# Optimization experiments

Hardware: AMD Instinct MI355X
Metric: run time of the kernel (lower is better)

The kernel has to match this reference:

```python
import jax, jax.numpy as jnp
import numpy as np

EMBED_DIM = 1024
NUM_HEADS = 16
HEAD_DIM = EMBED_DIM // NUM_HEADS
B, S = 2, 2048


def setup_inputs() -> dict:
    key = jax.random.key(0)
    ks = jax.random.split(key, 9)
    d = EMBED_DIM
    scale = 1.0 / np.sqrt(d)
    inp = {
        "x": jax.random.normal(ks[0], (B, S, d), dtype=jnp.float32),
        "mask": jnp.ones((B, S), dtype=jnp.int32),
        "Wq": jax.random.normal(ks[1], (d, d), dtype=jnp.float32) * scale,
        "bq": jnp.zeros((d,), dtype=jnp.float32),
        "Wk": jax.random.normal(ks[2], (d, d), dtype=jnp.float32) * scale,
        "bk": jnp.zeros((d,), dtype=jnp.float32),
        "Wv": jax.random.normal(ks[3], (d, d), dtype=jnp.float32) * scale,
        "bv": jnp.zeros((d,), dtype=jnp.float32),
        "Wo": jax.random.normal(ks[4], (d, d), dtype=jnp.float32) * scale,
        "bo": jnp.zeros((d,), dtype=jnp.float32),
    }
    return inp


def reference(x, mask, Wq, bq, Wk, bk, Wv, bv, Wo, bo):
    b, s, _ = x.shape
    # projections; torch Linear computes x @ W.T + b
    q = (x @ Wq.T + bq).reshape(b, s, NUM_HEADS, HEAD_DIM).transpose(0, 2, 1, 3)
    k = (x @ Wk.T + bk).reshape(b, s, NUM_HEADS, HEAD_DIM).transpose(0, 2, 1, 3)
    v = (x @ Wv.T + bv).reshape(b, s, NUM_HEADS, HEAD_DIM).transpose(0, 2, 1, 3)
    scores = jnp.einsum("bhqd,bhkd->bhqk", q, k) / np.sqrt(HEAD_DIM)  # (B,H,S,S)
    m = (mask == 0)[:, None, None, :]  # broadcast over heads and query pos
    scores = jnp.where(m, jnp.float32(-1e9), scores)
    attn = jax.nn.softmax(scores, axis=-1)
    out = jnp.einsum("bhqk,bhkd->bhqd", attn, v)
    out = out.transpose(0, 2, 1, 3).reshape(b, s, EMBED_DIM)
    return out @ Wo.T + bo
```

## Files before the change

kernel.cpp:

```cpp
#include <hip/hip_runtime.h>

#define EMBED 1024
#define NHEAD 16
#define HDIM  64
#define BB    2
#define SS    2048

typedef __bf16 bf16x8 __attribute__((ext_vector_type(8)));
typedef float  f32x4  __attribute__((ext_vector_type(4)));
typedef _Float16 f16x8 __attribute__((ext_vector_type(8)));
typedef __fp16 hf16x2 __attribute__((ext_vector_type(2)));
typedef unsigned short u16x8 __attribute__((ext_vector_type(8)));

#if defined(__has_builtin)
#if __has_builtin(__builtin_amdgcn_exp2f)
#define EXP2(x) __builtin_amdgcn_exp2f(x)
#else
#define EXP2(x) exp2f(x)
#endif
#else
#define EXP2(x) exp2f(x)
#endif

__device__ __forceinline__ unsigned short f2bf(float f) {
  union { float f; unsigned u; } v; v.f = f;
  unsigned r = v.u + 0x7fffu + ((v.u >> 16) & 1u);
  return (unsigned short)(r >> 16);
}

__device__ __forceinline__ float bf2f(unsigned short u) {
  union { unsigned u; float f; } v; v.u = ((unsigned)u) << 16;
  return v.f;
}

__device__ __forceinline__ unsigned short f2h(float f) {
  union { _Float16 h; unsigned short u; } t;
  t.h = (_Float16)f;
  return t.u;
}

__device__ __forceinline__ void g2l16(const unsigned short* g, unsigned short* l) {
  __builtin_amdgcn_global_load_lds(
      (const __attribute__((address_space(1))) unsigned int*)g,
      (__attribute__((address_space(3))) unsigned int*)l, 16, 0, 0);
}

__global__ __launch_bounds__(256)
void cvt5_kernel(const float* __restrict__ x,  const float* __restrict__ Wq,
                 const float* __restrict__ Wk, const float* __restrict__ Wv,
                 const float* __restrict__ Wo, const int* __restrict__ mask,
                 unsigned short* __restrict__ xb,  unsigned short* __restrict__ Wqb,
                 unsigned short* __restrict__ Wkb, unsigned short* __restrict__ Wvb,
                 unsigned short* __restrict__ Wob, float* __restrict__ mbias) {
  const int i = blockIdx.x * 256 + threadIdx.x;
  if (i < (1 << 21)) {
    const float* src;
    unsigned short* dst;
    int j;
    if (i < (1 << 20)) {
      src = x; dst = xb; j = i;
    } else {
      const int t = i - (1 << 20);
      const int r = t >> 18;
      j = t & ((1 << 18) - 1);
      src = (r == 0) ? Wq : (r == 1) ? Wk : (r == 2) ? Wv : Wo;
      dst = (r == 0) ? Wqb : (r == 1) ? Wkb : (r == 2) ? Wvb : Wob;
    }
    const float4 f = ((const float4*)src)[j];
    ushort4 u;
    u.x = f2bf(f.x); u.y = f2bf(f.y); u.z = f2bf(f.z); u.w = f2bf(f.w);
    ((ushort4*)dst)[j] = u;
  } else {
    const int j = i - (1 << 21);
    const int4 m = ((const int4*)mask)[j];
    float4 o;
    o.x = m.x ? 0.f : -1e30f; o.y = m.y ? 0.f : -1e30f;
    o.z = m.z ? 0.f : -1e30f; o.w = m.w ? 0.f : -1e30f;
    ((float4*)mbias)[j] = o;
  }
}

template <typename EpiFn>
__device__ __forceinline__
void gemm_core(const unsigned short* __restrict__ A,
               const unsigned short* __restrict__ Bm,
               int m0, int n0, EpiFn epi) {
  __shared__ unsigned short sA[128 * 64];
  __shared__ unsigned short sB[128 * 64];
  const int tid = threadIdx.x;
  const int l  = tid & 63;
  const int w  = tid >> 6;
  const int lm = l & 15;
  const int qd = l >> 4;
  const int wm = w & 1;
  const int wn = w >> 1;

  f32x4 acc[4][4];
#pragma unroll
  for (int i = 0; i < 4; ++i)
#pragma unroll
    for (int j = 0; j < 4; ++j) acc[i][j] = (f32x4){0.f, 0.f, 0.f, 0.f};

  for (int k0 = 0; k0 < EMBED; k0 += 64) {
#pragma unroll
    for (int i = 0; i < 4; ++i) {
      const int t = i * 256 + tid;
      const int r = t >> 3;
      const int c = (t & 7) ^ (r & 7);
      g2l16(A + (m0 + r) * EMBED + k0 + c * 8, &sA[(i * 256 + (w << 6)) * 8]);
      g2l16(Bm + (n0 + r) * EMBED + k0 + c * 8, &sB[(i * 256 + (w << 6)) * 8]);
    }
    __syncthreads();
#pragma unroll
    for (int kk = 0; kk < 2; ++kk) {
      bf16x8 af[4], bfr[4];
#pragma unroll
      for (int mi = 0; mi < 4; ++mi) {
        const int R = wm * 64 + mi * 16 + lm;
        const int ch = R * 8 + (((kk << 2) + qd) ^ (R & 7));
        af[mi] = *(const bf16x8*)&sA[ch * 8];
      }
#pragma unroll
      for (int ni = 0; ni < 4; ++ni) {
        const int R = wn * 64 + ni * 16 + lm;
        const int ch = R * 8 + (((kk << 2) + qd) ^ (R & 7));
        bfr[ni] = *(const bf16x8*)&sB[ch * 8];
      }
#pragma unroll
      for (int mi = 0; mi < 4; ++mi)
#pragma unroll
        for (int ni = 0; ni < 4; ++ni)
          acc[mi][ni] = __builtin_amdgcn_mfma_f32_16x16x32_bf16(
              af[mi], bfr[ni], acc[mi][ni], 0, 0, 0);
    }
    __syncthreads();
  }

#pragma unroll
  for (int mi = 0; mi < 4; ++mi)
#pragma unroll
    for (int ni = 0; ni < 4; ++ni) {
      const int mb = m0 + wm * 64 + mi * 16 + qd * 4;
      const int n  = n0 + wn * 64 + ni * 16 + lm;
      epi(acc[mi][ni], mb, n);
    }
}

__device__ __forceinline__ void decode_tile(int flat, int& a0, int& b0) {
  const int sub = flat & 15;
  const int g = flat >> 4;
  a0 = ((g >> 2) * 2 + (sub >> 3));
  b0 = ((g & 3) * 8 + (sub & 7));
}

__global__ __launch_bounds__(256)
void gemm_qkv(const unsigned short* __restrict__ xb,
              const unsigned short* __restrict__ Wqb,
              const unsigned short* __restrict__ Wkb,
              const unsigned short* __restrict__ Wvb,
              const float* __restrict__ bq, const float* __restrict__ bk,
              const float* __restrict__ bv,
              unsigned short* __restrict__ Qb, unsigned short* __restrict__ Kb,
              unsigned short* __restrict__ VTb) {
  const int z = blockIdx.y;
  int a0, b0;
  decode_tile(blockIdx.x, a0, b0);
  if (z < 2) {
    const unsigned short* A = z ? Wkb : Wqb;
    const float* bias = z ? bk : bq;
    unsigned short* O = z ? Kb : Qb;
    const float scale = z ? 1.0f : 0.125f * 1.4426950408889634f;
    gemm_core(A, xb, a0 * 128, b0 * 128, [&](const f32x4& v, int mb, int n) {
      const float4 bvv = *(const float4*)&bias[mb];
      const int h = mb >> 6, d0 = mb & 63;
      const int b = n >> 11, s = n & 2047;
      int sw = s;
      if (z == 1)
        sw = (s & ~31) | (((s >> 2) & 1) << 4) | (((s >> 3) & 3) << 2) | (s & 3);
      ushort4 u;
      u.x = f2bf((v.x + bvv.x) * scale); u.y = f2bf((v.y + bvv.y) * scale);
      u.z = f2bf((v.z + bvv.z) * scale); u.w = f2bf((v.w + bvv.w) * scale);
      *(ushort4*)&O[(((b * NHEAD + h) * SS) + sw) * HDIM + d0] = u;
    });
  } else {
    gemm_core(xb, Wvb, b0 * 128, a0 * 128, [&](const f32x4& v, int mb, int n) {
      const float bvv = bv[n];
      const int b = mb >> 11, s = mb & 2047;
      const int h = n >> 6, d = n & 63;
      ushort4 u;
      u.x = f2h(v.x + bvv); u.y = f2h(v.y + bvv);
      u.z = f2h(v.z + bvv); u.w = f2h(v.w + bvv);
      *(ushort4*)&VTb[(((b * NHEAD + h) * HDIM) + d) * SS + s] = u;
    });
  }
}

__global__ __launch_bounds__(256)
void gemm_out(const unsigned short* __restrict__ Wob,
              const unsigned short* __restrict__ Opart,
              const float* __restrict__ Lpart,
              const float* __restrict__ bo, float* __restrict__ out) {
  __shared__ unsigned short sA[128 * 64];
  __shared__ unsigned short sB[128 * 64];
  int a0, b0;
  decode_tile(blockIdx.x, a0, b0);
  const int m0 = a0 * 128, n0 = b0 * 128;
  const int tid = threadIdx.x;
  const int l  = tid & 63;
  const int w  = tid >> 6;
  const int lm = l & 15;
  const int qd = l >> 4;
  const int wm = w & 1;
  const int wn = w >> 1;

  f32x4 acc[4][4];
#pragma unroll
  for (int i = 0; i < 4; ++i)
#pragma unroll
    for (int j = 0; j < 4; ++j) acc[i][j] = (f32x4){0.f, 0.f, 0.f, 0.f};

  for (int k0 = 0; k0 < EMBED; k0 += 64) {
    const int h = k0 >> 6;
#pragma unroll
    for (int i = 0; i < 4; ++i) {
      const int t = i * 256 + tid;
      const int r = t >> 3;
      const int c = (t & 7) ^ (r & 7);
      g2l16(Wob + (m0 + r) * EMBED + k0 + c * 8, &sA[(i * 256 + (w << 6)) * 8]);
    }
#pragma unroll
    for (int i = 0; i < 4; ++i) {
      const int t = i * 256 + tid;
      const int r = t >> 3;
      const int c = (t & 7) ^ (r & 7);
      const int n = n0 + r;
      const int bb = n >> 11, q = n & 2047;
      const int lidx = (bb * NHEAD + h) * SS + q;
      const float rinv = 1.f / (Lpart[lidx] + Lpart[BB * NHEAD * SS + lidx]);
      const u16x8 pa = *(const u16x8*)&Opart[n * EMBED + k0 + c * 8];
      const u16x8 pb =
          *(const u16x8*)&Opart[BB * SS * EMBED + n * EMBED + k0 + c * 8];
      u16x8 o;
#pragma unroll
      for (int e = 0; e < 8; ++e)
        o[e] = f2bf((bf2f(pa[e]) + bf2f(pb[e])) * rinv);
      *(u16x8*)&sB[(i * 256 + tid) * 8] = o;
    }
    __syncthreads();
#pragma unroll
    for (int kk = 0; kk < 2; ++kk) {
      bf16x8 af[4], bfr[4];
#pragma unroll
      for (int mi = 0; mi < 4; ++mi) {
        const int R = wm * 64 + mi * 16 + lm;
        const int ch = R * 8 + (((kk << 2) + qd) ^ (R & 7));
        af[mi] = *(const bf16x8*)&sA[ch * 8];
      }
#pragma unroll
      for (int ni = 0; ni < 4; ++ni) {
        const int R = wn * 64 + ni * 16 + lm;
        const int ch = R * 8 + (((kk << 2) + qd) ^ (R & 7));
        bfr[ni] = *(const bf16x8*)&sB[ch * 8];
      }
#pragma unroll
      for (int mi = 0; mi < 4; ++mi)
#pragma unroll
        for (int ni = 0; ni < 4; ++ni)
          acc[mi][ni] = __builtin_amdgcn_mfma_f32_16x16x32_bf16(
              af[mi], bfr[ni], acc[mi][ni], 0, 0, 0);
    }
    __syncthreads();
  }

#pragma unroll
  for (int mi = 0; mi < 4; ++mi)
#pragma unroll
    for (int ni = 0; ni < 4; ++ni) {
      const int mb = m0 + wm * 64 + mi * 16 + qd * 4;
      const int n  = n0 + wn * 64 + ni * 16 + lm;
      const float4 bvv = *(const float4*)&bo[mb];
      float4 o;
      o.x = acc[mi][ni][0] + bvv.x; o.y = acc[mi][ni][1] + bvv.y;
      o.z = acc[mi][ni][2] + bvv.z; o.w = acc[mi][ni][3] + bvv.w;
      *(float4*)&out[n * EMBED + mb] = o;
    }
}

__global__ __launch_bounds__(256, 6)
void attn_kernel(const unsigned short* __restrict__ Q,
                 const unsigned short* __restrict__ K,
                 const unsigned short* __restrict__ VT,
                 const float* __restrict__ mbias,
                 unsigned short* __restrict__ Opart,
                 float* __restrict__ Lpart) {
  __shared__ unsigned short sK[64 * 64];
  __shared__ unsigned short sV[64 * 64];
  __shared__ float sMB[SS / 2];
  const int tid = threadIdx.x;
  const int l = tid & 63, w = tid >> 6;
  const int lm = l & 15, qd = l >> 4;
  const int b = blockIdx.z & 1, sp = blockIdx.z >> 1, h = blockIdx.y;
  const int q0 = blockIdx.x * 64 + w * 16;
  const unsigned short* Qh = Q + ((b * NHEAD + h) * SS) * HDIM;
  const unsigned short* Kh = K + ((b * NHEAD + h) * SS) * HDIM;
  const unsigned short* Vh = VT + ((b * NHEAD + h) * HDIM) * SS;
  const float* mb = mbias + b * SS + sp * (SS / 2);
  unsigned short* Op = Opart + sp * (BB * SS * EMBED);
  float* Lp = Lpart + sp * (BB * NHEAD * SS);
  const int kb0 = sp * (SS / 2);

  bf16x8 qf[2];
  qf[0] = *(const bf16x8*)&Qh[(q0 + lm) * HDIM + qd * 8];
  qf[1] = *(const bf16x8*)&Qh[(q0 + lm) * HDIM + 32 + qd * 8];

  auto stageKV = [&](int kb) {
#pragma unroll
    for (int i = 0; i < 2; ++i) {
      const int t = i * 256 + tid;
      const int r = t >> 3;
      const int c = (t & 7) ^ (r & 7);
      g2l16(Kh + (kb + r) * HDIM + c * 8, &sK[(i * 256 + (w << 6)) * 8]);
      g2l16(Vh + r * SS + kb + c * 8, &sV[(i * 256 + (w << 6)) * 8]);
    }
  };

  g2l16((const unsigned short*)(mb + tid * 4), (unsigned short*)&sMB[w * 256]);

  f32x4 Od[4];
#pragma unroll
  for (int i = 0; i < 4; ++i) Od[i] = (f32x4){0.f, 0.f, 0.f, 0.f};
  float lsum = 0.f;

  const int NT = (SS / 2) / 64;
  for (int t = 0; t < NT; ++t) {
    stageKV(kb0 + t * 64);
    __syncthreads();

#pragma unroll
    for (int p = 0; p < 2; ++p) {
      union PK { hf16x2 h2[4]; f16x8 v; } pk;
#pragma unroll
      for (int jj = 0; jj < 2; ++jj) {
        const int j = p * 2 + jj;
        const int R = j * 16 + lm;
        const bf16x8 k0 = *(const bf16x8*)&sK[(R * 8 + (qd ^ (lm & 7))) * 8];
        const bf16x8 k1 = *(const bf16x8*)&sK[(R * 8 + ((4 + qd) ^ (lm & 7))) * 8];
        const float4 bj = *(const float4*)&sMB[t * 64 + p * 32 + qd * 8 + jj * 4];
        f32x4 t0 = (f32x4){bj.x, bj.y, bj.z, bj.w};
        __builtin_amdgcn_s_setprio(1);
        t0 = __builtin_amdgcn_mfma_f32_16x16x32_bf16(k0, qf[0], t0, 0, 0, 0);
        t0 = __builtin_amdgcn_mfma_f32_16x16x32_bf16(k1, qf[1], t0, 0, 0, 0);
        __builtin_amdgcn_s_setprio(0);
        const float p0 = EXP2(t0[0]);
        const float p1 = EXP2(t0[1]);
        const float p2 = EXP2(t0[2]);
        const float p3 = EXP2(t0[3]);
        lsum += (p0 + p1) + (p2 + p3);
        pk.h2[jj * 2] = __builtin_amdgcn_cvt_pkrtz(p0, p1);
        pk.h2[jj * 2 + 1] = __builtin_amdgcn_cvt_pkrtz(p2, p3);
      }
      const f16x8 pf8 = pk.v;
      __builtin_amdgcn_s_setprio(1);
#pragma unroll
      for (int dt = 0; dt < 4; ++dt) {
        const f16x8 vf =
            *(const f16x8*)&sV[(dt * 16 + lm) * 64 + ((p * 4 + qd) ^ (lm & 7)) * 8];
        Od[dt] = __builtin_amdgcn_mfma_f32_16x16x32_f16(vf, pf8, Od[dt], 0, 0, 0);
      }
      __builtin_amdgcn_s_setprio(0);
    }
    __syncthreads();
  }

  float ls = lsum;
  ls += __shfl_xor(ls, 16);
  ls += __shfl_xor(ls, 32);
  if (qd == 0) Lp[(b * NHEAD + h) * SS + q0 + lm] = ls;
#pragma unroll
  for (int dt = 0; dt < 4; ++dt) {
    ushort4 u;
    u.x = f2bf(Od[dt][0]); u.y = f2bf(Od[dt][1]);
    u.z = f2bf(Od[dt][2]); u.w = f2bf(Od[dt][3]);
    *(ushort4*)&Op[(b * SS + q0 + lm) * EMBED + h * HDIM + dt * 16 + qd * 4] = u;
  }
}

extern "C" void kernel_launch(void* const* d_in, const int* in_sizes, int n_in,
                              void* d_out, int out_size, void* d_ws, size_t ws_size,
                              hipStream_t stream) {
  const float* x  = (const float*)d_in[0];
  const int* mask = (const int*)d_in[1];
  const float* Wq = (const float*)d_in[2];
  const float* bq = (const float*)d_in[3];
  const float* Wk = (const float*)d_in[4];
  const float* bk = (const float*)d_in[5];
  const float* Wv = (const float*)d_in[6];
  const float* bv = (const float*)d_in[7];
  const float* Wo = (const float*)d_in[8];
  const float* bo = (const float*)d_in[9];
  float* out = (float*)d_out;

  char* ws = (char*)d_ws;
  const size_t MB = 1024 * 1024;
  unsigned short* xb  = (unsigned short*)(ws);
  unsigned short* Wqb = (unsigned short*)(ws + 8 * MB);
  unsigned short* Wkb = Wqb + 1024 * 1024;
  unsigned short* Wvb = Wkb + 1024 * 1024;
  unsigned short* Wob = Wvb + 1024 * 1024;
  unsigned short* Qb  = (unsigned short*)(ws + 16 * MB);
  unsigned short* Kb  = (unsigned short*)(ws + 24 * MB);
  unsigned short* VTb = (unsigned short*)(ws + 32 * MB);
  unsigned short* Opart = (unsigned short*)(ws + 40 * MB);
  float* mbb   = (float*)(ws + 56 * MB);
  float* Lpart = (float*)(ws + 56 * MB + 64 * 1024);

  cvt5_kernel<<<8196, 256, 0, stream>>>(x, Wq, Wk, Wv, Wo, mask,
                                        xb, Wqb, Wkb, Wvb, Wob, mbb);
  gemm_qkv<<<dim3(256, 3), 256, 0, stream>>>(xb, Wqb, Wkb, Wvb, bq, bk, bv,
                                             Qb, Kb, VTb);
  attn_kernel<<<dim3(32, 16, 4), 256, 0, stream>>>(Qb, Kb, VTb, mbb,
                                                   Opart, Lpart);
  gemm_out<<<256, 256, 0, stream>>>(Wob, Opart, Lpart, bo, out);
}
```

Measured before the change: 227.0 us.

## Split split-K combine out of output GEMM and shrink its M tile

The split-K partial attention outputs are now combined and normalized in a separate elementwise kernel that writes a bf16 buffer (reusing the xb workspace). The output GEMM then loads that buffer with async global-to-LDS copies instead of doing register-level combining inside its K loop. Its tile shrinks from 128x128 to 64x128 and the grid doubles to 512 blocks for better CU occupancy. This adds a kernel launch and an extra round trip to global memory for the combined buffer.

```diff
diff --git a/kernel.cpp b/kernel.cpp
--- a/kernel.cpp
+++ b/kernel.cpp
@@ -10,7 +10,6 @@
 typedef float  f32x4  __attribute__((ext_vector_type(4)));
 typedef _Float16 f16x8 __attribute__((ext_vector_type(8)));
 typedef __fp16 hf16x2 __attribute__((ext_vector_type(2)));
-typedef unsigned short u16x8 __attribute__((ext_vector_type(8)));
 
 #if defined(__has_builtin)
 #if __has_builtin(__builtin_amdgcn_exp2f)
@@ -197,14 +196,12 @@
 
 __global__ __launch_bounds__(256)
 void gemm_out(const unsigned short* __restrict__ Wob,
-              const unsigned short* __restrict__ Opart,
-              const float* __restrict__ Lpart,
+              const unsigned short* __restrict__ Ob,
               const float* __restrict__ bo, float* __restrict__ out) {
-  __shared__ unsigned short sA[128 * 64];
+  __shared__ unsigned short sA[64 * 64];
   __shared__ unsigned short sB[128 * 64];
-  int a0, b0;
-  decode_tile(blockIdx.x, a0, b0);
-  const int m0 = a0 * 128, n0 = b0 * 128;
+  const int m0 = (blockIdx.x & 15) * 64;
+  const int n0 = (blockIdx.x >> 4) * 128;
   const int tid = threadIdx.x;
   const int l  = tid & 63;
   const int w  = tid >> 6;
@@ -213,46 +210,34 @@
   const int wm = w & 1;
   const int wn = w >> 1;
 
-  f32x4 acc[4][4];
-#pragma unroll
-  for (int i = 0; i < 4; ++i)
+  f32x4 acc[2][4];
+#pragma unroll
+  for (int i = 0; i < 2; ++i)
 #pragma unroll
     for (int j = 0; j < 4; ++j) acc[i][j] = (f32x4){0.f, 0.f, 0.f, 0.f};
 
   for (int k0 = 0; k0 < EMBED; k0 += 64) {
-    const int h = k0 >> 6;
+#pragma unroll
+    for (int i = 0; i < 2; ++i) {
+      const int t = i * 256 + tid;
+      const int r = t >> 3;
+      const int c = (t & 7) ^ (r & 7);
+      g2l16(Wob + (m0 + r) * EMBED + k0 + c * 8, &sA[(i * 256 + (w << 6)) * 8]);
+    }
 #pragma unroll
     for (int i = 0; i < 4; ++i) {
       const int t = i * 256 + tid;
       const int r = t >> 3;
       const int c = (t & 7) ^ (r & 7);
-      g2l16(Wob + (m0 + r) * EMBED + k0 + c * 8, &sA[(i * 256 + (w << 6)) * 8]);
-    }
-#pragma unroll
-    for (int i = 0; i < 4; ++i) {
-      const int t = i * 256 + tid;
-      const int r = t >> 3;
-      const int c = (t & 7) ^ (r & 7);
-      const int n = n0 + r;
-      const int bb = n >> 11, q = n & 2047;
-      const int lidx = (bb * NHEAD + h) * SS + q;
-      const float rinv = 1.f / (Lpart[lidx] + Lpart[BB * NHEAD * SS + lidx]);
-      const u16x8 pa = *(const u16x8*)&Opart[n * EMBED + k0 + c * 8];
-      const u16x8 pb =
-          *(const u16x8*)&Opart[BB * SS * EMBED + n * EMBED + k0 + c * 8];
-      u16x8 o;
-#pragma unroll
-      for (int e = 0; e < 8; ++e)
-        o[e] = f2bf((bf2f(pa[e]) + bf2f(pb[e])) * rinv);
-      *(u16x8*)&sB[(i * 256 + tid) * 8] = o;
+      g2l16(Ob + (n0 + r) * EMBED + k0 + c * 8, &sB[(i * 256 + (w << 6)) * 8]);
     }
     __syncthreads();
 #pragma unroll
     for (int kk = 0; kk < 2; ++kk) {
-      bf16x8 af[4], bfr[4];
-#pragma unroll
-      for (int mi = 0; mi < 4; ++mi) {
-        const int R = wm * 64 + mi * 16 + lm;
+      bf16x8 af[2], bfr[4];
+#pragma unroll
+      for (int mi = 0; mi < 2; ++mi) {
+        const int R = wm * 32 + mi * 16 + lm;
         const int ch = R * 8 + (((kk << 2) + qd) ^ (R & 7));
         af[mi] = *(const bf16x8*)&sA[ch * 8];
       }
@@ -263,7 +248,7 @@
         bfr[ni] = *(const bf16x8*)&sB[ch * 8];
       }
 #pragma unroll
-      for (int mi = 0; mi < 4; ++mi)
+      for (int mi = 0; mi < 2; ++mi)
 #pragma unroll
         for (int ni = 0; ni < 4; ++ni)
           acc[mi][ni] = __builtin_amdgcn_mfma_f32_16x16x32_bf16(
@@ -273,10 +258,10 @@
   }
 
 #pragma unroll
-  for (int mi = 0; mi < 4; ++mi)
+  for (int mi = 0; mi < 2; ++mi)
 #pragma unroll
     for (int ni = 0; ni < 4; ++ni) {
-      const int mb = m0 + wm * 64 + mi * 16 + qd * 4;
+      const int mb = m0 + wm * 32 + mi * 16 + qd * 4;
       const int n  = n0 + wn * 64 + ni * 16 + lm;
       const float4 bvv = *(const float4*)&bo[mb];
       float4 o;
@@ -385,6 +370,33 @@
   }
 }
 
+__global__ __launch_bounds__(256)
+void combine_kernel(const unsigned short* __restrict__ Opart,
+                    const float* __restrict__ Lpart,
+                    unsigned short* __restrict__ Ob) {
+  const int i = blockIdx.x * 256 + threadIdx.x;
+  const int base = i * 8;
+  const int token = base >> 10;
+  const int h = (base >> 6) & 15;
+  const int b = token >> 11, q = token & 2047;
+  const int lidx = (b * NHEAD + h) * SS + q;
+  const float ls = Lpart[lidx] + Lpart[BB * NHEAD * SS + lidx];
+  const float rinv = 1.f / ls;
+  const ushort4* p0 = (const ushort4*)&Opart[base];
+  const ushort4* p1 = (const ushort4*)&Opart[BB * SS * EMBED + base];
+  ushort4 o[2];
+#pragma unroll
+  for (int k = 0; k < 2; ++k) {
+    const ushort4 a = p0[k], c = p1[k];
+    o[k].x = f2bf((bf2f(a.x) + bf2f(c.x)) * rinv);
+    o[k].y = f2bf((bf2f(a.y) + bf2f(c.y)) * rinv);
+    o[k].z = f2bf((bf2f(a.z) + bf2f(c.z)) * rinv);
+    o[k].w = f2bf((bf2f(a.w) + bf2f(c.w)) * rinv);
+  }
+  *(ushort4*)&Ob[base] = o[0];
+  *(ushort4*)&Ob[base + 4] = o[1];
+}
+
 extern "C" void kernel_launch(void* const* d_in, const int* in_sizes, int n_in,
                               void* d_out, int out_size, void* d_ws, size_t ws_size,
                               hipStream_t stream) {
@@ -403,6 +415,7 @@
   char* ws = (char*)d_ws;
   const size_t MB = 1024 * 1024;
   unsigned short* xb  = (unsigned short*)(ws);
+  unsigned short* Ob  = (unsigned short*)(ws);
   unsigned short* Wqb = (unsigned short*)(ws + 8 * MB);
   unsigned short* Wkb = Wqb + 1024 * 1024;
   unsigned short* Wvb = Wkb + 1024 * 1024;
@@ -420,5 +433,6 @@
                                              Qb, Kb, VTb);
   attn_kernel<<<dim3(32, 16, 4), 256, 0, stream>>>(Qb, Kb, VTb, mbb,
                                                    Opart, Lpart);
-  gemm_out<<<256, 256, 0, stream>>>(Wob, Opart, Lpart, bo, out);
-}
+  combine_kernel<<<2048, 256, 0, stream>>>(Opart, Lpart, Ob);
+  gemm_out<<<512, 256, 0, stream>>>(Wob, Ob, bo, out);
+}
```

After: 207.0 us. 1.1x faster.
